# Performance work log

Hardware: AMD Instinct MI355X
Metric: run time of the kernel (lower is better)

Reference implementation:

```python
import jax, jax.numpy as jnp
import numpy as np

L1 = 1536
L2 = 15
L3 = 64
COUNT = 8
B = 16384


def setup_inputs() -> dict:
    key = jax.random.key(0)
    ks = jax.random.split(key, 10)
    d_in = 2 * L1 // 2  # 1536
    s1 = 1.0 / np.sqrt(d_in)
    s2 = 1.0 / np.sqrt(2 * L2)
    s3 = 1.0 / np.sqrt(L3)
    return {
        "x": jax.random.normal(ks[0], (B, d_in), dtype=jnp.float32),
        "ls_indices": jax.random.randint(ks[1], (B,), 0, COUNT, dtype=jnp.int32),
        "W1": jax.random.uniform(ks[2], (COUNT * (L2 + 1), d_in), jnp.float32, -s1, s1),
        "b1": jax.random.uniform(ks[3], (COUNT * (L2 + 1),), jnp.float32, -s1, s1),
        "Wf": jax.random.uniform(ks[4], (L2 + 1, d_in), jnp.float32, -s1, s1),
        "bf": jax.random.uniform(ks[5], (L2 + 1,), jnp.float32, -s1, s1),
        "W2": jax.random.uniform(ks[6], (COUNT * L3, 2 * L2), jnp.float32, -s2, s2),
        "b2": jax.random.uniform(ks[7], (COUNT * L3,), jnp.float32, -s2, s2),
        "Wo": jax.random.uniform(ks[8], (COUNT, L3), jnp.float32, -s3, s3),
        "bo": jax.random.uniform(ks[9], (COUNT,), jnp.float32, -s3, s3),
    }


def reference(x, ls_indices, W1, b1, Wf, bf, W2, b2, Wo, bo):
    count = Wo.shape[0]
    n = x.shape[0]
    idx = ls_indices[:, None, None]  # [B,1,1] selects the per-sample stack

    # l1: all stacks, then gather selected stack row per sample
    l1s = (x @ W1.T + b1).reshape(n, count, L2 + 1)          # [B, count, 16]
    l1f = x @ Wf.T + bf                                       # [B, 16]
    l1c = jnp.take_along_axis(l1s, idx, axis=1)[:, 0]         # [B, 16]

    l1c_, l1c_out = l1c[:, :L2], l1c[:, L2:]                  # [B,15], [B,1]
    l1f_, l1f_out = l1f[:, :L2], l1f[:, L2:]
    l1x = l1c_ + l1f_
    # squared-clipped-ReLU concat: [pow(x,2)*127/128, x] clamped to [0,1]
    l1x = jnp.clip(jnp.concatenate([l1x * l1x * (127.0 / 128.0), l1x], axis=1), 0.0, 1.0)  # [B,30]

    l2s = (l1x @ W2.T + b2).reshape(n, count, L3)             # [B, count, 64]
    l2c = jnp.take_along_axis(l2s, idx, axis=1)[:, 0]         # [B, 64]
    l2x = jnp.clip(l2c, 0.0, 1.0)

    l3s = (l2x @ Wo.T + bo).reshape(n, count, 1)              # [B, count, 1]
    l3c = jnp.take_along_axis(l3s, idx, axis=1)[:, 0]         # [B, 1]
    return l3c + l1f_out + l1c_out
```

## Files before the change

### kernel.cpp

```cpp
#include <hip/hip_runtime.h>
#include <hip/hip_bf16.h>
#include <stdint.h>

#define L1DIM  1536
#define NOUT   144
#define NSPLIT 8
#define KSPL   192
#define KSTEPS 6
#define KOCT   24
#define ROWS   16384
#define RT     16
#define NRT    1024
#define BLKS   64
#define PCOLS  32

typedef __bf16 bf16;
typedef __bf16 bf16x8 __attribute__((ext_vector_type(8)));
typedef float  floatx4 __attribute__((ext_vector_type(4)));

__global__ void pack_weights(const float* __restrict__ W1,
                             const float* __restrict__ Wf,
                             bf16* __restrict__ pw) {
    int t = blockIdx.x * blockDim.x + threadIdx.x;
    if (t >= NOUT * 192) return;
    int n = t / 192;
    int o = t % 192;
    const float* src = (n < 128) ? (W1 + (size_t)n * L1DIM + o * 8)
                                 : (Wf + (size_t)(n - 128) * L1DIM + o * 8);
    float4 s0 = ((const float4*)src)[0];
    float4 s1 = ((const float4*)src)[1];
    bf16x8 v;
    v[0] = (bf16)s0.x; v[1] = (bf16)s0.y; v[2] = (bf16)s0.z; v[3] = (bf16)s0.w;
    v[4] = (bf16)s1.x; v[5] = (bf16)s1.y; v[6] = (bf16)s1.z; v[7] = (bf16)s1.w;
    int spl = o / KOCT, ol = o % KOCT;
    *(bf16x8*)(pw + (((size_t)spl * KOCT + ol) * NOUT + n) * 8) = v;
}

__device__ __forceinline__ void gload_lds16(const void* g, void* l) {
    __builtin_amdgcn_global_load_lds(
        (const __attribute__((address_space(1))) void*)g,
        (__attribute__((address_space(3))) void*)l, 16, 0, 0);
}

__device__ __forceinline__ bf16x8 cvt8(float4 a, float4 b) {
    bf16x8 r;
    r[0] = (bf16)a.x; r[1] = (bf16)a.y; r[2] = (bf16)a.z; r[3] = (bf16)a.w;
    r[4] = (bf16)b.x; r[5] = (bf16)b.y; r[6] = (bf16)b.z; r[7] = (bf16)b.w;
    return r;
}

__global__ __launch_bounds__(512, 4) void gemm_l1(
    const float* __restrict__ x, const int* __restrict__ lsidx,
    const bf16* __restrict__ pw, float* __restrict__ pt)
{
    __shared__ bf16 lb[KOCT * NOUT * 8];

    const int tid  = threadIdx.x;
    const int wv   = tid >> 6;
    const int ln   = tid & 63;
    const int quad = ln >> 4;
    const int lm   = ln & 15;

    const int q   = blockIdx.x >> 6;
    const int blk = blockIdx.x & 63;

    {
        const bf16* src = pw + (size_t)q * KOCT * NOUT * 8;
        for (int c = tid; c < KOCT * NOUT; c += 512)
            gload_lds16(src + (size_t)c * 8, &lb[(size_t)c * 8]);
    }
    __syncthreads();

    const int rA = (blk * 16 + wv) * RT;
    const int rB = (blk * 16 + 8 + wv) * RT;

    const float* xa = x + (size_t)(rA + lm) * L1DIM + q * KSPL;
    const float* xb = x + (size_t)(rB + lm) * L1DIM + q * KSPL;

    floatx4 accA[9], accB[9];
#pragma unroll
    for (int i = 0; i < 9; i++) {
        accA[i] = (floatx4){0.f, 0.f, 0.f, 0.f};
        accB[i] = (floatx4){0.f, 0.f, 0.f, 0.f};
    }

    float4 pa0 = *(const float4*)(xa + quad * 8);
    float4 pa1 = *(const float4*)(xa + quad * 8 + 4);
    float4 pb0 = *(const float4*)(xb + quad * 8);
    float4 pb1 = *(const float4*)(xb + quad * 8 + 4);

    for (int s = 0; s < KSTEPS; s++) {
        bf16x8 afA = cvt8(pa0, pa1);
        bf16x8 afB = cvt8(pb0, pb1);
        if (s < KSTEPS - 1) {
            const float* na = xa + (s + 1) * 32 + quad * 8;
            pa0 = *(const float4*)na;
            pa1 = *(const float4*)(na + 4);
            const float* nb = xb + (s + 1) * 32 + quad * 8;
            pb0 = *(const float4*)nb;
            pb1 = *(const float4*)(nb + 4);
        }
        const bf16* lbase = &lb[((size_t)(s * 4 + quad) * NOUT) * 8];
#pragma unroll
        for (int t = 0; t < 9; t++) {
            bf16x8 bfrag = *(const bf16x8*)&lbase[(t * 16 + lm) * 8];
            accA[t] = __builtin_amdgcn_mfma_f32_16x16x32_bf16(afA, bfrag, accA[t], 0, 0, 0);
            accB[t] = __builtin_amdgcn_mfma_f32_16x16x32_bf16(afB, bfrag, accB[t], 0, 0, 0);
        }
    }

#pragma unroll
    for (int u = 0; u < 2; u++) {
        const floatx4* acc = u ? accB : accA;
        const int r0 = u ? rB : rA;
#pragma unroll
        for (int rp = 0; rp < 4; rp++) {
            const int row = r0 + quad * 4 + rp;
            const int bkt = lsidx[row];
            float c = acc[0][rp];
#pragma unroll
            for (int t = 1; t < 8; t++) c = (bkt == t) ? acc[t][rp] : c;
            const float f = acc[8][rp];
            float* dst = pt + ((size_t)q * ROWS + row) * PCOLS;
            dst[lm]      = c;
            dst[16 + lm] = f;
        }
    }
}

__global__ __launch_bounds__(256) void epilogue(
    const float* __restrict__ pt, const int* __restrict__ lsidx,
    const float* __restrict__ b1, const float* __restrict__ bf_,
    const float* __restrict__ W2, const float* __restrict__ b2,
    const float* __restrict__ Wo, const float* __restrict__ bo,
    float* __restrict__ out)
{
    __shared__ float ep[32][33];

    const int tid = threadIdx.x;
    const int er  = tid >> 3;
    const int sub = tid & 7;
    const int row = blockIdx.x * 32 + er;

    float4 s = {0.f, 0.f, 0.f, 0.f};
#pragma unroll
    for (int q = 0; q < NSPLIT; q++) {
        float4 v = *(const float4*)&pt[((size_t)q * ROWS + row) * PCOLS + sub * 4];
        s.x += v.x; s.y += v.y; s.z += v.z; s.w += v.w;
    }
    *(float4*)&ep[er][sub * 4] = s;
    __syncthreads();

    const int bkt = lsidx[row];
    const float l1c15 = ep[er][15] + b1[bkt * 16 + 15];
    const float l1f15 = ep[er][31] + bf_[15];

    float l1x[30];
#pragma unroll
    for (int j = 0; j < 15; j++) {
        float tj = (ep[er][j] + b1[bkt * 16 + j]) + (ep[er][16 + j] + bf_[j]);
        float sq = tj * tj * (127.0f / 128.0f);
        l1x[j]      = fminf(fmaxf(sq, 0.f), 1.f);
        l1x[15 + j] = fminf(fmaxf(tj, 0.f), 1.f);
    }

    float part = 0.f;
#pragma unroll
    for (int o = 0; o < 8; o++) {
        const int oi = bkt * 64 + sub * 8 + o;
        const float2* wrow = (const float2*)(W2 + oi * 30);
        float a = b2[oi];
#pragma unroll
        for (int j2 = 0; j2 < 15; j2++) {
            float2 w = wrow[j2];
            a += l1x[2 * j2] * w.x + l1x[2 * j2 + 1] * w.y;
        }
        a = fminf(fmaxf(a, 0.f), 1.f);
        part += a * Wo[oi];
    }
    part += __shfl_xor(part, 1);
    part += __shfl_xor(part, 2);
    part += __shfl_xor(part, 4);
    if (sub == 0) out[row] = part + bo[bkt] + l1c15 + l1f15;
}

extern "C" void kernel_launch(void* const* d_in, const int* in_sizes, int n_in,
                              void* d_out, int out_size, void* d_ws, size_t ws_size,
                              hipStream_t stream) {
    const float* x   = (const float*)d_in[0];
    const int*   idx = (const int*)  d_in[1];
    const float* W1  = (const float*)d_in[2];
    const float* b1  = (const float*)d_in[3];
    const float* Wf  = (const float*)d_in[4];
    const float* bf  = (const float*)d_in[5];
    const float* W2  = (const float*)d_in[6];
    const float* b2  = (const float*)d_in[7];
    const float* Wo  = (const float*)d_in[8];
    const float* bo  = (const float*)d_in[9];
    float* out = (float*)d_out;

    float* pt = (float*)d_ws;
    bf16*  pw = (bf16*)((char*)d_ws + (size_t)NSPLIT * ROWS * PCOLS * 4);

    pack_weights<<<dim3((NOUT * 192 + 255) / 256), dim3(256), 0, stream>>>(W1, Wf, pw);
    gemm_l1<<<dim3(NSPLIT * BLKS), dim3(512), 0, stream>>>(x, idx, pw, pt);
    epilogue<<<dim3(ROWS / 32), dim3(256), 0, stream>>>(pt, idx, b1, bf, W2, b2, Wo, bo, out);
}
```

Baseline: 192.6 us.

## Stage x rows through LDS and stream bf16 weights from global with prefetch

Cuts the K split from 8 to 2, so fewer partial sums are written to the workspace and read back by the epilogue. Each wave loads its 16 rows of x in coalesced 256-column chunks into a padded per-wave LDS buffer, double-buffered in registers. Weight fragments are no longer kept in LDS; each wave reads them from global memory into registers and prefetches one step ahead. The large per-wave LDS footprint limits each CU to one block, and every wave rereads the whole weight slice through cache, which adds L2 traffic and lowers occupancy.

```diff
diff --git a/kernel.cpp b/kernel.cpp
--- a/kernel.cpp
+++ b/kernel.cpp
@@ -4,14 +4,13 @@
 
 #define L1DIM  1536
 #define NOUT   144
-#define NSPLIT 8
-#define KSPL   192
-#define KSTEPS 6
-#define KOCT   24
+#define NSPLIT 2
+#define KSPL   768
+#define CHUNK  256
+#define NCHNK  3
+#define STEPS  24
+#define LROW   260
 #define ROWS   16384
-#define RT     16
-#define NRT    1024
-#define BLKS   64
 #define PCOLS  32
 
 typedef __bf16 bf16;
@@ -32,14 +31,7 @@
     bf16x8 v;
     v[0] = (bf16)s0.x; v[1] = (bf16)s0.y; v[2] = (bf16)s0.z; v[3] = (bf16)s0.w;
     v[4] = (bf16)s1.x; v[5] = (bf16)s1.y; v[6] = (bf16)s1.z; v[7] = (bf16)s1.w;
-    int spl = o / KOCT, ol = o % KOCT;
-    *(bf16x8*)(pw + (((size_t)spl * KOCT + ol) * NOUT + n) * 8) = v;
-}
-
-__device__ __forceinline__ void gload_lds16(const void* g, void* l) {
-    __builtin_amdgcn_global_load_lds(
-        (const __attribute__((address_space(1))) void*)g,
-        (__attribute__((address_space(3))) void*)l, 16, 0, 0);
+    *(bf16x8*)(pw + ((size_t)o * NOUT + n) * 8) = v;
 }
 
 __device__ __forceinline__ bf16x8 cvt8(float4 a, float4 b) {
@@ -49,11 +41,11 @@
     return r;
 }
 
-__global__ __launch_bounds__(512, 4) void gemm_l1(
+__global__ __launch_bounds__(512, 2) void gemm_l1(
     const float* __restrict__ x, const int* __restrict__ lsidx,
     const bf16* __restrict__ pw, float* __restrict__ pt)
 {
-    __shared__ bf16 lb[KOCT * NOUT * 8];
+    __shared__ float law[8][16][LROW];
 
     const int tid  = threadIdx.x;
     const int wv   = tid >> 6;
@@ -61,70 +53,80 @@
     const int quad = ln >> 4;
     const int lm   = ln & 15;
 
-    const int q   = blockIdx.x >> 6;
-    const int blk = blockIdx.x & 63;
+    const int q   = blockIdx.x >> 7;
+    const int blk = blockIdx.x & 127;
+    const int rA  = blk * 128 + wv * 16;
+
+    const float* xbase = x + (size_t)rA * L1DIM + q * KSPL;
+    float* lw = &law[wv][0][0];
 
     {
-        const bf16* src = pw + (size_t)q * KOCT * NOUT * 8;
-        for (int c = tid; c < KOCT * NOUT; c += 512)
-            gload_lds16(src + (size_t)c * 8, &lb[(size_t)c * 8]);
-    }
-    __syncthreads();
-
-    const int rA = (blk * 16 + wv) * RT;
-    const int rB = (blk * 16 + 8 + wv) * RT;
-
-    const float* xa = x + (size_t)(rA + lm) * L1DIM + q * KSPL;
-    const float* xb = x + (size_t)(rB + lm) * L1DIM + q * KSPL;
-
-    floatx4 accA[9], accB[9];
-#pragma unroll
-    for (int i = 0; i < 9; i++) {
-        accA[i] = (floatx4){0.f, 0.f, 0.f, 0.f};
-        accB[i] = (floatx4){0.f, 0.f, 0.f, 0.f};
-    }
-
-    float4 pa0 = *(const float4*)(xa + quad * 8);
-    float4 pa1 = *(const float4*)(xa + quad * 8 + 4);
-    float4 pb0 = *(const float4*)(xb + quad * 8);
-    float4 pb1 = *(const float4*)(xb + quad * 8 + 4);
-
-    for (int s = 0; s < KSTEPS; s++) {
-        bf16x8 afA = cvt8(pa0, pa1);
-        bf16x8 afB = cvt8(pb0, pb1);
-        if (s < KSTEPS - 1) {
-            const float* na = xa + (s + 1) * 32 + quad * 8;
-            pa0 = *(const float4*)na;
-            pa1 = *(const float4*)(na + 4);
-            const float* nb = xb + (s + 1) * 32 + quad * 8;
-            pb0 = *(const float4*)nb;
-            pb1 = *(const float4*)(nb + 4);
-        }
-        const bf16* lbase = &lb[((size_t)(s * 4 + quad) * NOUT) * 8];
-#pragma unroll
-        for (int t = 0; t < 9; t++) {
-            bf16x8 bfrag = *(const bf16x8*)&lbase[(t * 16 + lm) * 8];
-            accA[t] = __builtin_amdgcn_mfma_f32_16x16x32_bf16(afA, bfrag, accA[t], 0, 0, 0);
-            accB[t] = __builtin_amdgcn_mfma_f32_16x16x32_bf16(afB, bfrag, accB[t], 0, 0, 0);
-        }
-    }
-
-#pragma unroll
-    for (int u = 0; u < 2; u++) {
-        const floatx4* acc = u ? accB : accA;
-        const int r0 = u ? rB : rA;
-#pragma unroll
-        for (int rp = 0; rp < 4; rp++) {
-            const int row = r0 + quad * 4 + rp;
-            const int bkt = lsidx[row];
-            float c = acc[0][rp];
-#pragma unroll
-            for (int t = 1; t < 8; t++) c = (bkt == t) ? acc[t][rp] : c;
-            const float f = acc[8][rp];
-            float* dst = pt + ((size_t)q * ROWS + row) * PCOLS;
-            dst[lm]      = c;
-            dst[16 + lm] = f;
-        }
+        float4 av[16];
+#pragma unroll
+        for (int r = 0; r < 16; r++)
+            av[r] = *(const float4*)(xbase + (size_t)r * L1DIM + ln * 4);
+#pragma unroll
+        for (int r = 0; r < 16; r++)
+            *(float4*)(lw + r * LROW + ln * 4) = av[r];
+    }
+
+    floatx4 acc[9];
+#pragma unroll
+    for (int i = 0; i < 9; i++) acc[i] = (floatx4){0.f, 0.f, 0.f, 0.f};
+
+    const bf16* pb0 = pw + (((size_t)q * 96 + quad) * NOUT + lm) * 8;
+    bf16x8 bcur[9];
+#pragma unroll
+    for (int t = 0; t < 9; t++)
+        bcur[t] = *(const bf16x8*)(pb0 + t * 16 * 8);
+
+    for (int c = 0; c < NCHNK; c++) {
+        float4 av2[16];
+        if (c < NCHNK - 1) {
+#pragma unroll
+            for (int r = 0; r < 16; r++)
+                av2[r] = *(const float4*)(xbase + (size_t)r * L1DIM
+                                          + (c + 1) * CHUNK + ln * 4);
+        }
+#pragma unroll
+        for (int s = 0; s < 8; s++) {
+            const int st = c * 8 + s;
+            bf16x8 bnxt[9];
+            if (st < STEPS - 1) {
+                const bf16* pn = pw + (((size_t)q * 96 + (st + 1) * 4 + quad) * NOUT + lm) * 8;
+#pragma unroll
+                for (int t = 0; t < 9; t++)
+                    bnxt[t] = *(const bf16x8*)(pn + t * 16 * 8);
+            }
+            const float* ap = lw + lm * LROW + s * 32 + quad * 8;
+            float4 a0 = *(const float4*)ap;
+            float4 a1 = *(const float4*)(ap + 4);
+            bf16x8 af = cvt8(a0, a1);
+#pragma unroll
+            for (int t = 0; t < 9; t++)
+                acc[t] = __builtin_amdgcn_mfma_f32_16x16x32_bf16(af, bcur[t], acc[t], 0, 0, 0);
+            if (st < STEPS - 1) {
+#pragma unroll
+                for (int t = 0; t < 9; t++) bcur[t] = bnxt[t];
+            }
+        }
+        if (c < NCHNK - 1) {
+#pragma unroll
+            for (int r = 0; r < 16; r++)
+                *(float4*)(lw + r * LROW + ln * 4) = av2[r];
+        }
+    }
+
+#pragma unroll
+    for (int rp = 0; rp < 4; rp++) {
+        const int row = rA + quad * 4 + rp;
+        const int bkt = lsidx[row];
+        float csel = acc[0][rp];
+#pragma unroll
+        for (int t = 1; t < 8; t++) csel = (bkt == t) ? acc[t][rp] : csel;
+        float* dst = pt + ((size_t)q * ROWS + row) * PCOLS;
+        dst[lm]      = csel;
+        dst[16 + lm] = acc[8][rp];
     }
 }
 
@@ -203,6 +205,6 @@
     bf16*  pw = (bf16*)((char*)d_ws + (size_t)NSPLIT * ROWS * PCOLS * 4);
 
     pack_weights<<<dim3((NOUT * 192 + 255) / 256), dim3(256), 0, stream>>>(W1, Wf, pw);
-    gemm_l1<<<dim3(NSPLIT * BLKS), dim3(512), 0, stream>>>(x, idx, pw, pt);
+    gemm_l1<<<dim3(NSPLIT * 128), dim3(512), 0, stream>>>(x, idx, pw, pt);
     epilogue<<<dim3(ROWS / 32), dim3(256), 0, stream>>>(pt, idx, b1, bf, W2, b2, Wo, bo, out);
 }
```

After: 208.3 us. 8.2% more time.
